# Kernel tuning notes

Measured on AMD Instinct MI355X. Metric: run time of the kernel, lower is better.

The kernel has to match this reference:

```python
import jax, jax.numpy as jnp
import numpy as np

N = 100000      # nodes
D = 128         # in_channels
P = 64          # num_prompts
E = 3_200_000   # graph edges
EPT = 5_000_000 # kNN prompt-graph edges (k=50)
EPS = 0.1       # ot_epsilon
ITERS = 20      # sinkhorn max_iters


def _l2norm(x):
    # F.normalize(p=2, dim=1) with eps=1e-12
    return x / jnp.maximum(jnp.linalg.norm(x, axis=1, keepdims=True), 1e-12)


def setup_inputs() -> dict:
    key = jax.random.key(0)
    k1, k2, k3, k4, k5 = jax.random.split(key, 5)
    x = jax.random.normal(k1, (N, D), dtype=jnp.float32)
    edge_index = jax.random.randint(k2, (2, E), 0, N, dtype=jnp.int32)
    edge_weight = jax.random.uniform(k3, (E,), dtype=jnp.float32)
    pt_edge_index = jax.random.randint(k4, (2, EPT), 0, N, dtype=jnp.int32)
    # xavier_uniform for prompt_tokens
    bound = float(np.sqrt(6.0 / (P + D)))
    prompt_tokens = jax.random.uniform(k5, (P, D), dtype=jnp.float32, minval=-bound, maxval=bound)
    alpha_feat = jnp.float32(0.01)
    gamma = jnp.float32(0.5)
    return {"x": x, "edge_index": edge_index, "edge_weight": edge_weight,
            "pt_edge_index": pt_edge_index, "prompt_tokens": prompt_tokens,
            "alpha_feat": alpha_feat, "gamma": gamma}


def reference(x, edge_index, edge_weight, pt_edge_index, prompt_tokens, alpha_feat, gamma):
    n = x.shape[0]
    row, col = edge_index[0], edge_index[1]
    # degree of col (unweighted count), GCN-style symmetric normalization
    deg = jax.ops.segment_sum(jnp.ones_like(edge_weight), col, num_segments=n)
    deg_inv_sqrt = jnp.where(deg > 0, deg ** -0.5, 0.0)
    norm_weight = deg_inv_sqrt[row] * edge_weight * deg_inv_sqrt[col]  # [E]
    # scatter-add aggregation: x_aggr[row] += x[col] * norm_weight
    x_aggr = jax.ops.segment_sum(x[col] * norm_weight[:, None], row, num_segments=n)
    x_struct = (1.0 - gamma) * x + gamma * x_aggr

    xs = _l2norm(x_struct)               # [N, D]
    pn = _l2norm(prompt_tokens)          # [P, D]

    # Sinkhorn OT: cost = 1 - cosine sim, uniform marginals
    C = 1.0 - xs @ pn.T                  # [N, P]
    K = jnp.exp(-C / EPS)
    p = prompt_tokens.shape[0]
    a = jnp.full((n,), 1.0 / n, dtype=x.dtype)
    b = jnp.full((p,), 1.0 / p, dtype=x.dtype)
    u = a
    for _ in range(ITERS):
        v = b / (K.T @ u + 1e-30)
        u = a / (K @ v + 1e-30)
    T_star = u[:, None] * K * v[None, :]  # [N, P]
    ot_loss = jnp.sum(T_star * C)

    prompt_message = n * (T_star @ prompt_tokens)  # [N, D]
    x_adapted = x + alpha_feat * prompt_message

    xf = _l2norm(x_adapted)
    pt_row, pt_col = pt_edge_index[0], pt_edge_index[1]
    w = jnp.sum(xf[pt_row] * xf[pt_col], axis=1)   # [EPT]
    w = jax.nn.relu(w)
    w = w / (jnp.max(w) + 1e-8)
    return (x_adapted, ot_loss, w)
```

## Files before the change

kernel.cpp:

```cpp
#include <hip/hip_runtime.h>
#include <stdint.h>

#define D_DIM 128
#define P_DIM 64

#define O_CNTR   0x000000ull
#define O_CNTC   0x080000ull
#define O_DIS    0x100000ull
#define O_ROWPTR 0x180000ull
#define O_CURSOR 0x200000ull
#define O_PART   0x280000ull
#define O_KT     0x290000ull
#define O_MAXW   0x2A0000ull
#define O_PNT    0x2B0000ull
#define O_U      0x300000ull
#define O_CSRC   0x400000ull
#define O_CSRW   0x1040000ull
#define O_XF     0x400000ull
#define O_K      0x1C80000ull

__device__ __forceinline__ float wsumf(float v){
  #pragma unroll
  for (int d=1; d<64; d<<=1) v += __shfl_xor(v, d);
  return v;
}

__device__ __forceinline__ unsigned f2bf(float f){
  unsigned u = __float_as_uint(f);
  return (u + 0x7fffu + ((u>>16)&1u)) >> 16;
}

__device__ __forceinline__ float dp2(unsigned a, unsigned b){
  float al = __uint_as_float(a<<16),  ah = __uint_as_float(a & 0xffff0000u);
  float bl = __uint_as_float(b<<16),  bh = __uint_as_float(b & 0xffff0000u);
  return al*bl + ah*bh;
}

__global__ void k_zero(int* cntr, int* cntc, float* kt, unsigned* maxw, float* loss_slot, int n){
  int i = blockIdx.x*blockDim.x + threadIdx.x;
  int st = gridDim.x*blockDim.x;
  for (int j=i; j<n; j+=st){ cntr[j]=0; cntc[j]=0; }
  for (int j=i; j<21*64; j+=st) kt[j]=0.f;
  if (i==0){ *maxw = 0u; *loss_slot = 0.f; }
}

__global__ void k_deg(const int* __restrict__ ei, int E, int* cntr, int* cntc){
  int i = blockIdx.x*blockDim.x + threadIdx.x;
  int st = gridDim.x*blockDim.x;
  for (int e=i; e<E; e+=st){
    atomicAdd(&cntr[ei[e]], 1);
    atomicAdd(&cntc[ei[E+e]], 1);
  }
}

__global__ void k_deginv(const int* __restrict__ cntc, float* __restrict__ dis, int n){
  int i = blockIdx.x*blockDim.x + threadIdx.x;
  if (i < n){
    int c = cntc[i];
    dis[i] = (c > 0) ? rsqrtf((float)c) : 0.f;
  }
}

__global__ void k_scan_a(const int* __restrict__ cnt, int* __restrict__ part, int n){
  __shared__ int sm[4];
  int base = blockIdx.x*1024;
  int t = threadIdx.x;
  int s = 0;
  #pragma unroll
  for (int k=0;k<4;k++){ int idx = base + t + 256*k; if (idx<n) s += cnt[idx]; }
  #pragma unroll
  for (int d=1; d<64; d<<=1) s += __shfl_xor(s, d);
  if ((t&63)==0) sm[t>>6] = s;
  __syncthreads();
  if (t==0) part[blockIdx.x] = sm[0]+sm[1]+sm[2]+sm[3];
}

__global__ void k_scan_b(int* part, int nb, int* row_ptr, int n, int E){
  if (threadIdx.x==0 && blockIdx.x==0){
    int run = 0;
    for (int i=0;i<nb;i++){ int v = part[i]; part[i] = run; run += v; }
    row_ptr[n] = E;
  }
}

__global__ void k_scan_c(const int* __restrict__ cnt, const int* __restrict__ part,
                         int* __restrict__ row_ptr, int* __restrict__ cursor, int n){
  __shared__ int warp_tot[4];
  int base = blockIdx.x*1024;
  int t = threadIdx.x;
  int lane = t&63, wv = t>>6;
  int v[4];
  #pragma unroll
  for (int k=0;k<4;k++){ int idx = base + t*4 + k; v[k] = (idx<n) ? cnt[idx] : 0; }
  int local = v[0]+v[1]+v[2]+v[3];
  int sc = local;
  #pragma unroll
  for (int d=1; d<64; d<<=1){ int y = __shfl_up(sc, d); if (lane>=d) sc += y; }
  if (lane==63) warp_tot[wv] = sc;
  __syncthreads();
  int woff = 0;
  for (int i=0;i<wv;i++) woff += warp_tot[i];
  int run = part[blockIdx.x] + woff + (sc - local);
  #pragma unroll
  for (int k=0;k<4;k++){
    int idx = base + t*4 + k;
    if (idx<n){ row_ptr[idx] = run; cursor[idx] = run; run += v[k]; }
  }
}

__global__ void k_prep_pn(const float* __restrict__ pt, float* __restrict__ pnT){
  int r = blockIdx.x;
  int l = threadIdx.x;
  float2 v = ((const float2*)pt)[r*64 + l];
  float ss = wsumf(v.x*v.x + v.y*v.y);
  float inv = 1.f / fmaxf(sqrtf(ss), 1e-12f);
  pnT[(2*l)*64   + r] = v.x*inv;
  pnT[(2*l+1)*64 + r] = v.y*inv;
}

__global__ void k_scatter(const int* __restrict__ ei, const float* __restrict__ ew,
                          const float* __restrict__ dis, int* cursor,
                          int* __restrict__ csr_col, float* __restrict__ csr_w, int E){
  int i = blockIdx.x*blockDim.x + threadIdx.x;
  int st = gridDim.x*blockDim.x;
  for (int e=i; e<E; e+=st){
    int r = ei[e], c = ei[E+e];
    float w = dis[r]*ew[e]*dis[c];
    int pos = atomicAdd(&cursor[r], 1);
    csr_col[pos] = c; csr_w[pos] = w;
  }
}

__global__ __launch_bounds__(256) void k_struct(const float* __restrict__ x,
    const int* __restrict__ row_ptr, const int* __restrict__ csr_col,
    const float* __restrict__ csr_w, const float* __restrict__ pnT_g,
    const float* __restrict__ gamma_p, float* __restrict__ Km, int n){
  __shared__ __align__(16) float pnT[128*64];
  __shared__ __align__(16) float xsrow[4][128];
  for (int i=threadIdx.x; i<128*64; i+=256) pnT[i] = pnT_g[i];
  __syncthreads();
  float g = *gamma_p, om = 1.f - g;
  int lane = threadIdx.x&63, wv = threadIdx.x>>6;
  int wid = blockIdx.x*4 + wv, nw = gridDim.x*4;
  for (int r=wid; r<n; r+=nw){
    int e0 = row_ptr[r], e1 = row_ptr[r+1];
    float ax=0.f, ay=0.f;
    for (int e=e0; e<e1; e++){
      int c = csr_col[e]; float w = csr_w[e];
      float2 xv = ((const float2*)x)[(size_t)c*64 + lane];
      ax = fmaf(w, xv.x, ax); ay = fmaf(w, xv.y, ay);
    }
    float2 xr = ((const float2*)x)[(size_t)r*64 + lane];
    float sx = om*xr.x + g*ax;
    float sy = om*xr.y + g*ay;
    float ss = wsumf(sx*sx + sy*sy);
    float inv = 1.f / fmaxf(sqrtf(ss), 1e-12f);
    xsrow[wv][2*lane]   = sx*inv;
    xsrow[wv][2*lane+1] = sy*inv;
    float acc = 0.f;
    #pragma unroll
    for (int d=0; d<128; d++) acc = fmaf(xsrow[wv][d], pnT[d*64+lane], acc);
    Km[(size_t)r*64 + lane] = exp2f((acc - 1.f) * 14.426950408889634f);
  }
}

__global__ __launch_bounds__(256) void k_colsum(const float* __restrict__ Km,
                                                float* __restrict__ kt_out, int n){
  __shared__ float ktsh[64];
  int tid = threadIdx.x;
  if (tid<64) ktsh[tid] = 0.f;
  __syncthreads();
  int lane = tid&63, wv = tid>>6, sub = lane>>4, li = lane&15;
  float4 acc = make_float4(0,0,0,0);
  int wid = blockIdx.x*4 + wv, nw = gridDim.x*4;
  for (int base=wid*4; base<n; base+=nw*4){
    int r = base + sub;
    if (r<n){
      float4 kv = ((const float4*)(Km + (size_t)r*64))[li];
      acc.x += kv.x; acc.y += kv.y; acc.z += kv.z; acc.w += kv.w;
    }
  }
  acc.x += __shfl_xor(acc.x,16); acc.x += __shfl_xor(acc.x,32);
  acc.y += __shfl_xor(acc.y,16); acc.y += __shfl_xor(acc.y,32);
  acc.z += __shfl_xor(acc.z,16); acc.z += __shfl_xor(acc.z,32);
  acc.w += __shfl_xor(acc.w,16); acc.w += __shfl_xor(acc.w,32);
  if (sub==0){
    atomicAdd(&ktsh[li*4+0], acc.x);
    atomicAdd(&ktsh[li*4+1], acc.y);
    atomicAdd(&ktsh[li*4+2], acc.z);
    atomicAdd(&ktsh[li*4+3], acc.w);
  }
  __syncthreads();
  float anorm = 1.0f/(float)n;
  if (tid<64) atomicAdd(&kt_out[tid], ktsh[tid]*anorm);
}

__global__ __launch_bounds__(256) void k_sink(const float* __restrict__ Km,
    const float* __restrict__ kt_in, float* __restrict__ kt_out,
    float* __restrict__ u, int n){
  __shared__ __align__(16) float vsh[64];
  __shared__ float ktsh[64];
  int tid = threadIdx.x;
  if (tid<64){ vsh[tid] = (1.0f/64.0f)/(kt_in[tid] + 1e-30f); ktsh[tid] = 0.f; }
  __syncthreads();
  int lane = tid&63, wv = tid>>6, sub = lane>>4, li = lane&15;
  float4 vv = ((const float4*)vsh)[li];
  float anorm = 1.0f/(float)n;
  float4 acc = make_float4(0,0,0,0);
  int wid = blockIdx.x*4 + wv, nw = gridDim.x*4;
  for (int base=wid*4; base<n; base+=nw*4){
    int r = base + sub;
    float4 kv = make_float4(0,0,0,0);
    if (r<n) kv = ((const float4*)(Km + (size_t)r*64))[li];
    float d = kv.x*vv.x + kv.y*vv.y + kv.z*vv.z + kv.w*vv.w;
    d += __shfl_xor(d,1); d += __shfl_xor(d,2); d += __shfl_xor(d,4); d += __shfl_xor(d,8);
    float un = anorm/(d + 1e-30f);
    if (li==0 && r<n) u[r] = un;
    acc.x = fmaf(kv.x, un, acc.x);
    acc.y = fmaf(kv.y, un, acc.y);
    acc.z = fmaf(kv.z, un, acc.z);
    acc.w = fmaf(kv.w, un, acc.w);
  }
  acc.x += __shfl_xor(acc.x,16); acc.x += __shfl_xor(acc.x,32);
  acc.y += __shfl_xor(acc.y,16); acc.y += __shfl_xor(acc.y,32);
  acc.z += __shfl_xor(acc.z,16); acc.z += __shfl_xor(acc.z,32);
  acc.w += __shfl_xor(acc.w,16); acc.w += __shfl_xor(acc.w,32);
  if (sub==0){
    atomicAdd(&ktsh[li*4+0], acc.x);
    atomicAdd(&ktsh[li*4+1], acc.y);
    atomicAdd(&ktsh[li*4+2], acc.z);
    atomicAdd(&ktsh[li*4+3], acc.w);
  }
  __syncthreads();
  if (tid<64) atomicAdd(&kt_out[tid], ktsh[tid]);
}

__global__ __launch_bounds__(256) void k_final(const float* __restrict__ x,
    const float* __restrict__ Km, const float* __restrict__ u,
    const float* __restrict__ kt19, const float* __restrict__ pt,
    const float* __restrict__ alpha_p, float* __restrict__ out_x,
    float* __restrict__ out_loss, unsigned* __restrict__ xf, int n){
  __shared__ __align__(16) float pts[64*128];
  __shared__ float trow[4][64];
  __shared__ float vsh[64];
  __shared__ float blockloss;
  int tid = threadIdx.x;
  for (int i=tid; i<8192; i+=256) pts[i] = pt[i];
  if (tid<64) vsh[tid] = (1.0f/64.0f)/(kt19[tid] + 1e-30f);
  if (tid==0) blockloss = 0.f;
  __syncthreads();
  float alpha = *alpha_p;
  float coeff = alpha*(float)n;
  int lane = tid&63, wv = tid>>6;
  int wid = blockIdx.x*4 + wv, nw = gridDim.x*4;
  float lossacc = 0.f;
  for (int r=wid; r<n; r+=nw){
    float kv = Km[(size_t)r*64 + lane];
    float T = u[r]*kv*vsh[lane];
    float C = log2f(kv) * (-0.069314718055994531f);
    lossacc = fmaf(T, C, lossacc);
    trow[wv][lane] = T;
    float m0=0.f, m1=0.f;
    #pragma unroll
    for (int p=0; p<64; p++){
      float t = trow[wv][p];
      float2 pv = ((const float2*)pts)[p*64 + lane];
      m0 = fmaf(t, pv.x, m0); m1 = fmaf(t, pv.y, m1);
    }
    float2 xr = ((const float2*)x)[(size_t)r*64 + lane];
    float ox = fmaf(coeff, m0, xr.x);
    float oy = fmaf(coeff, m1, xr.y);
    ((float2*)out_x)[(size_t)r*64 + lane] = make_float2(ox, oy);
    float ss = wsumf(ox*ox + oy*oy);
    float inv = 1.f / fmaxf(sqrtf(ss), 1e-12f);
    unsigned lo = f2bf(ox*inv), hi = f2bf(oy*inv);
    xf[(size_t)r*64 + lane] = lo | (hi<<16);
  }
  lossacc = wsumf(lossacc);
  if (lane==0) atomicAdd(&blockloss, lossacc);
  __syncthreads();
  if (tid==0) atomicAdd(out_loss, blockloss);
}

__global__ __launch_bounds__(256) void k_edge(const int* __restrict__ pte,
    const unsigned* __restrict__ xf, float* __restrict__ wout,
    unsigned* __restrict__ maxw, int ept){
  __shared__ unsigned blockmax;
  if (threadIdx.x==0) blockmax = 0u;
  __syncthreads();
  int lane = threadIdx.x&63, wv = threadIdx.x>>6, sub = lane>>4, li = lane&15;
  int wid = blockIdx.x*4 + wv, nw = gridDim.x*4;
  float lm = 0.f;
  for (int base=wid*4; base<ept; base+=nw*4){
    int e = base + sub;
    float dot = 0.f;
    if (e<ept){
      int r = pte[e], c = pte[ept+e];
      uint4 A = *(((const uint4*)(xf + (size_t)r*64)) + li);
      uint4 B = *(((const uint4*)(xf + (size_t)c*64)) + li);
      dot = dp2(A.x,B.x) + dp2(A.y,B.y) + dp2(A.z,B.z) + dp2(A.w,B.w);
    }
    dot += __shfl_xor(dot,1); dot += __shfl_xor(dot,2);
    dot += __shfl_xor(dot,4); dot += __shfl_xor(dot,8);
    if (li==0 && e<ept){
      float w = fmaxf(dot, 0.f);
      wout[e] = w;
      lm = fmaxf(lm, w);
    }
  }
  #pragma unroll
  for (int d=1; d<64; d<<=1) lm = fmaxf(lm, __shfl_xor(lm, d));
  if (lane==0) atomicMax(&blockmax, __float_as_uint(lm));
  __syncthreads();
  if (threadIdx.x==0) atomicMax(maxw, blockmax);
}

__global__ void k_normw(float* __restrict__ w, const unsigned* __restrict__ maxw, int ept){
  float inv = 1.f/(__uint_as_float(*maxw) + 1e-8f);
  int i = blockIdx.x*blockDim.x + threadIdx.x;
  int st = gridDim.x*blockDim.x;
  for (int e=i; e<ept; e+=st) w[e] *= inv;
}

extern "C" void kernel_launch(void* const* d_in, const int* in_sizes, int n_in,
                              void* d_out, int out_size, void* d_ws, size_t ws_size,
                              hipStream_t stream){
  const float* x       = (const float*)d_in[0];
  const int*   ei      = (const int*)  d_in[1];
  const float* ew      = (const float*)d_in[2];
  const int*   pte     = (const int*)  d_in[3];
  const float* pt      = (const float*)d_in[4];
  const float* alpha_p = (const float*)d_in[5];
  const float* gamma_p = (const float*)d_in[6];
  int n   = in_sizes[0] / D_DIM;
  int E   = in_sizes[1] / 2;
  int ept = in_sizes[3] / 2;

  char* ws = (char*)d_ws;
  int*      cntr    = (int*)     (ws + O_CNTR);
  int*      cntc    = (int*)     (ws + O_CNTC);
  float*    dis     = (float*)   (ws + O_DIS);
  int*      row_ptr = (int*)     (ws + O_ROWPTR);
  int*      cursor  = (int*)     (ws + O_CURSOR);
  int*      part    = (int*)     (ws + O_PART);
  float*    kt      = (float*)   (ws + O_KT);
  unsigned* maxw    = (unsigned*)(ws + O_MAXW);
  float*    pnT     = (float*)   (ws + O_PNT);
  float*    ubuf    = (float*)   (ws + O_U);
  int*      csrc    = (int*)     (ws + O_CSRC);
  float*    csrw    = (float*)   (ws + O_CSRW);
  unsigned* xf      = (unsigned*)(ws + O_XF);
  float*    Km      = (float*)   (ws + O_K);

  float* out_x    = (float*)d_out;
  float* out_loss = (float*)d_out + (size_t)n*D_DIM;
  float* out_w    = out_loss + 1;

  int nb = (n + 1023)/1024;

  k_zero   <<<512, 256, 0, stream>>>(cntr, cntc, kt, maxw, out_loss, n);
  k_deg    <<<2048, 256, 0, stream>>>(ei, E, cntr, cntc);
  k_deginv <<<(n+255)/256, 256, 0, stream>>>(cntc, dis, n);
  k_scan_a <<<nb, 256, 0, stream>>>(cntr, part, n);
  k_scan_b <<<1, 64, 0, stream>>>(part, nb, row_ptr, n, E);
  k_scan_c <<<nb, 256, 0, stream>>>(cntr, part, row_ptr, cursor, n);
  k_prep_pn<<<64, 64, 0, stream>>>(pt, pnT);
  k_scatter<<<2048, 256, 0, stream>>>(ei, ew, dis, cursor, csrc, csrw, E);
  k_struct <<<2048, 256, 0, stream>>>(x, row_ptr, csrc, csrw, pnT, gamma_p, Km, n);
  k_colsum <<<1024, 256, 0, stream>>>(Km, kt, n);
  for (int t=1; t<=20; t++)
    k_sink <<<1024, 256, 0, stream>>>(Km, kt + (t-1)*64, kt + t*64, ubuf, n);
  k_final  <<<2048, 256, 0, stream>>>(x, Km, ubuf, kt + 19*64, pt, alpha_p,
                                      out_x, out_loss, xf, n);
  k_edge   <<<4096, 256, 0, stream>>>(pte, xf, out_w, maxw, ept);
  k_normw  <<<2048, 256, 0, stream>>>(out_w, maxw, ept);
}
```

Before: 2.167 ms.

## Fuse column sum into struct kernel, interleave CSR, bf16 prompts, XCD-local row partitioning

```diff
diff --git a/kernel.cpp b/kernel.cpp
--- a/kernel.cpp
+++ b/kernel.cpp
@@ -12,10 +12,9 @@
 #define O_PART   0x280000ull
 #define O_KT     0x290000ull
 #define O_MAXW   0x2A0000ull
-#define O_PNT    0x2B0000ull
+#define O_PNB    0x2B0000ull
 #define O_U      0x300000ull
-#define O_CSRC   0x400000ull
-#define O_CSRW   0x1040000ull
+#define O_CSR    0x400000ull
 #define O_XF     0x400000ull
 #define O_K      0x1C80000ull
 
@@ -30,10 +29,11 @@
   return (u + 0x7fffu + ((u>>16)&1u)) >> 16;
 }
 
+__device__ __forceinline__ float bflo(unsigned u){ return __uint_as_float(u<<16); }
+__device__ __forceinline__ float bfhi(unsigned u){ return __uint_as_float(u & 0xffff0000u); }
+
 __device__ __forceinline__ float dp2(unsigned a, unsigned b){
-  float al = __uint_as_float(a<<16),  ah = __uint_as_float(a & 0xffff0000u);
-  float bl = __uint_as_float(b<<16),  bh = __uint_as_float(b & 0xffff0000u);
-  return al*bl + ah*bh;
+  return bflo(a)*bflo(b) + bfhi(a)*bfhi(b);
 }
 
 __global__ void k_zero(int* cntr, int* cntc, float* kt, unsigned* maxw, float* loss_slot, int n){
@@ -108,49 +108,68 @@
   }
 }
 
-__global__ void k_prep_pn(const float* __restrict__ pt, float* __restrict__ pnT){
+__global__ void k_prep_pn(const float* __restrict__ pt, unsigned* __restrict__ pnb){
   int r = blockIdx.x;
   int l = threadIdx.x;
   float2 v = ((const float2*)pt)[r*64 + l];
   float ss = wsumf(v.x*v.x + v.y*v.y);
   float inv = 1.f / fmaxf(sqrtf(ss), 1e-12f);
-  pnT[(2*l)*64   + r] = v.x*inv;
-  pnT[(2*l+1)*64 + r] = v.y*inv;
+  pnb[l*64 + r] = f2bf(v.x*inv) | (f2bf(v.y*inv) << 16);
 }
 
 __global__ void k_scatter(const int* __restrict__ ei, const float* __restrict__ ew,
                           const float* __restrict__ dis, int* cursor,
-                          int* __restrict__ csr_col, float* __restrict__ csr_w, int E){
+                          uint2* __restrict__ csr, int E){
   int i = blockIdx.x*blockDim.x + threadIdx.x;
   int st = gridDim.x*blockDim.x;
   for (int e=i; e<E; e+=st){
     int r = ei[e], c = ei[E+e];
     float w = dis[r]*ew[e]*dis[c];
     int pos = atomicAdd(&cursor[r], 1);
-    csr_col[pos] = c; csr_w[pos] = w;
+    csr[pos] = make_uint2((unsigned)c, __float_as_uint(w));
   }
 }
 
 __global__ __launch_bounds__(256) void k_struct(const float* __restrict__ x,
-    const int* __restrict__ row_ptr, const int* __restrict__ csr_col,
-    const float* __restrict__ csr_w, const float* __restrict__ pnT_g,
-    const float* __restrict__ gamma_p, float* __restrict__ Km, int n){
-  __shared__ __align__(16) float pnT[128*64];
+    const int* __restrict__ row_ptr, const uint2* __restrict__ csr,
+    const unsigned* __restrict__ pnb_g, const float* __restrict__ gamma_p,
+    float* __restrict__ Km, float* __restrict__ kt0, int n){
+  __shared__ unsigned pnbs[64*64];
   __shared__ __align__(16) float xsrow[4][128];
-  for (int i=threadIdx.x; i<128*64; i+=256) pnT[i] = pnT_g[i];
+  __shared__ float ktsh[64];
+  int tid = threadIdx.x;
+  for (int i=tid; i<4096; i+=256) pnbs[i] = pnb_g[i];
+  if (tid<64) ktsh[tid] = 0.f;
   __syncthreads();
   float g = *gamma_p, om = 1.f - g;
-  int lane = threadIdx.x&63, wv = threadIdx.x>>6;
+  int lane = tid&63, wv = tid>>6;
   int wid = blockIdx.x*4 + wv, nw = gridDim.x*4;
+  const float2* X2 = (const float2*)x;
+  float kacc = 0.f;
   for (int r=wid; r<n; r+=nw){
     int e0 = row_ptr[r], e1 = row_ptr[r+1];
     float ax=0.f, ay=0.f;
-    for (int e=e0; e<e1; e++){
-      int c = csr_col[e]; float w = csr_w[e];
-      float2 xv = ((const float2*)x)[(size_t)c*64 + lane];
+    int e = e0;
+    for (; e+3 < e1; e += 4){
+      uint2 q0 = csr[e], q1 = csr[e+1], q2 = csr[e+2], q3 = csr[e+3];
+      float2 v0 = X2[(size_t)q0.x*64 + lane];
+      float2 v1 = X2[(size_t)q1.x*64 + lane];
+      float2 v2 = X2[(size_t)q2.x*64 + lane];
+      float2 v3 = X2[(size_t)q3.x*64 + lane];
+      float w0 = __uint_as_float(q0.y), w1 = __uint_as_float(q1.y);
+      float w2 = __uint_as_float(q2.y), w3 = __uint_as_float(q3.y);
+      ax = fmaf(w0, v0.x, ax); ay = fmaf(w0, v0.y, ay);
+      ax = fmaf(w1, v1.x, ax); ay = fmaf(w1, v1.y, ay);
+      ax = fmaf(w2, v2.x, ax); ay = fmaf(w2, v2.y, ay);
+      ax = fmaf(w3, v3.x, ax); ay = fmaf(w3, v3.y, ay);
+    }
+    for (; e < e1; e++){
+      uint2 q = csr[e];
+      float2 xv = X2[(size_t)q.x*64 + lane];
+      float w = __uint_as_float(q.y);
       ax = fmaf(w, xv.x, ax); ay = fmaf(w, xv.y, ay);
     }
-    float2 xr = ((const float2*)x)[(size_t)r*64 + lane];
+    float2 xr = X2[(size_t)r*64 + lane];
     float sx = om*xr.x + g*ax;
     float sy = om*xr.y + g*ay;
     float ss = wsumf(sx*sx + sy*sy);
@@ -159,40 +178,19 @@
     xsrow[wv][2*lane+1] = sy*inv;
     float acc = 0.f;
     #pragma unroll
-    for (int d=0; d<128; d++) acc = fmaf(xsrow[wv][d], pnT[d*64+lane], acc);
-    Km[(size_t)r*64 + lane] = exp2f((acc - 1.f) * 14.426950408889634f);
-  }
-}
-
-__global__ __launch_bounds__(256) void k_colsum(const float* __restrict__ Km,
-                                                float* __restrict__ kt_out, int n){
-  __shared__ float ktsh[64];
-  int tid = threadIdx.x;
-  if (tid<64) ktsh[tid] = 0.f;
-  __syncthreads();
-  int lane = tid&63, wv = tid>>6, sub = lane>>4, li = lane&15;
-  float4 acc = make_float4(0,0,0,0);
-  int wid = blockIdx.x*4 + wv, nw = gridDim.x*4;
-  for (int base=wid*4; base<n; base+=nw*4){
-    int r = base + sub;
-    if (r<n){
-      float4 kv = ((const float4*)(Km + (size_t)r*64))[li];
-      acc.x += kv.x; acc.y += kv.y; acc.z += kv.z; acc.w += kv.w;
-    }
-  }
-  acc.x += __shfl_xor(acc.x,16); acc.x += __shfl_xor(acc.x,32);
-  acc.y += __shfl_xor(acc.y,16); acc.y += __shfl_xor(acc.y,32);
-  acc.z += __shfl_xor(acc.z,16); acc.z += __shfl_xor(acc.z,32);
-  acc.w += __shfl_xor(acc.w,16); acc.w += __shfl_xor(acc.w,32);
-  if (sub==0){
-    atomicAdd(&ktsh[li*4+0], acc.x);
-    atomicAdd(&ktsh[li*4+1], acc.y);
-    atomicAdd(&ktsh[li*4+2], acc.z);
-    atomicAdd(&ktsh[li*4+3], acc.w);
-  }
-  __syncthreads();
-  float anorm = 1.0f/(float)n;
-  if (tid<64) atomicAdd(&kt_out[tid], ktsh[tid]*anorm);
+    for (int k=0; k<64; k++){
+      unsigned pp = pnbs[k*64 + lane];
+      float2 xv = *(const float2*)&xsrow[wv][2*k];
+      acc = fmaf(bflo(pp), xv.x, acc);
+      acc = fmaf(bfhi(pp), xv.y, acc);
+    }
+    float kv = exp2f((acc - 1.f) * 14.426950408889634f);
+    Km[(size_t)r*64 + lane] = kv;
+    kacc += kv;
+  }
+  atomicAdd(&ktsh[lane], kacc);
+  __syncthreads();
+  if (tid<64) atomicAdd(&kt0[tid], ktsh[tid] * (1.0f/(float)n));
 }
 
 __global__ __launch_bounds__(256) void k_sink(const float* __restrict__ Km,
@@ -207,15 +205,17 @@
   float4 vv = ((const float4*)vsh)[li];
   float anorm = 1.0f/(float)n;
   float4 acc = make_float4(0,0,0,0);
-  int wid = blockIdx.x*4 + wv, nw = gridDim.x*4;
-  for (int base=wid*4; base<n; base+=nw*4){
+  int xcd = blockIdx.x & 7, lb = blockIdx.x >> 3, nlb = gridDim.x >> 3;
+  int r0 = (int)((long long)xcd*n/8), r1 = (int)((long long)(xcd+1)*n/8);
+  int wid = lb*4 + wv, nw = nlb*4;
+  for (int base=r0+wid*4; base<r1; base+=nw*4){
     int r = base + sub;
     float4 kv = make_float4(0,0,0,0);
-    if (r<n) kv = ((const float4*)(Km + (size_t)r*64))[li];
+    if (r<r1) kv = ((const float4*)(Km + (size_t)r*64))[li];
     float d = kv.x*vv.x + kv.y*vv.y + kv.z*vv.z + kv.w*vv.w;
     d += __shfl_xor(d,1); d += __shfl_xor(d,2); d += __shfl_xor(d,4); d += __shfl_xor(d,8);
     float un = anorm/(d + 1e-30f);
-    if (li==0 && r<n) u[r] = un;
+    if (li==0 && r<r1) u[r] = un;
     acc.x = fmaf(kv.x, un, acc.x);
     acc.y = fmaf(kv.y, un, acc.y);
     acc.z = fmaf(kv.z, un, acc.z);
@@ -252,9 +252,11 @@
   float alpha = *alpha_p;
   float coeff = alpha*(float)n;
   int lane = tid&63, wv = tid>>6;
-  int wid = blockIdx.x*4 + wv, nw = gridDim.x*4;
+  int xcd = blockIdx.x & 7, lb = blockIdx.x >> 3, nlb = gridDim.x >> 3;
+  int r0 = (int)((long long)xcd*n/8), r1 = (int)((long long)(xcd+1)*n/8);
+  int wid = lb*4 + wv, nw = nlb*4;
   float lossacc = 0.f;
-  for (int r=wid; r<n; r+=nw){
+  for (int r=r0+wid; r<r1; r+=nw){
     float kv = Km[(size_t)r*64 + lane];
     float T = u[r]*kv*vsh[lane];
     float C = log2f(kv) * (-0.069314718055994531f);
@@ -291,21 +293,31 @@
   int lane = threadIdx.x&63, wv = threadIdx.x>>6, sub = lane>>4, li = lane&15;
   int wid = blockIdx.x*4 + wv, nw = gridDim.x*4;
   float lm = 0.f;
-  for (int base=wid*4; base<ept; base+=nw*4){
-    int e = base + sub;
-    float dot = 0.f;
-    if (e<ept){
-      int r = pte[e], c = pte[ept+e];
-      uint4 A = *(((const uint4*)(xf + (size_t)r*64)) + li);
-      uint4 B = *(((const uint4*)(xf + (size_t)c*64)) + li);
-      dot = dp2(A.x,B.x) + dp2(A.y,B.y) + dp2(A.z,B.z) + dp2(A.w,B.w);
-    }
-    dot += __shfl_xor(dot,1); dot += __shfl_xor(dot,2);
-    dot += __shfl_xor(dot,4); dot += __shfl_xor(dot,8);
-    if (li==0 && e<ept){
-      float w = fmaxf(dot, 0.f);
-      wout[e] = w;
-      lm = fmaxf(lm, w);
+  for (int base=wid*8; base<ept; base+=nw*8){
+    int eA = base + sub, eB = base + 4 + sub;
+    bool vA = eA < ept, vB = eB < ept;
+    float dA = 0.f, dB = 0.f;
+    uint4 A0, A1, B0, B1;
+    int rA=0,cA=0,rB=0,cB=0;
+    if (vA){ rA = pte[eA]; cA = pte[ept+eA]; }
+    if (vB){ rB = pte[eB]; cB = pte[ept+eB]; }
+    if (vA){
+      A0 = *(((const uint4*)(xf + (size_t)rA*64)) + li);
+      A1 = *(((const uint4*)(xf + (size_t)cA*64)) + li);
+    }
+    if (vB){
+      B0 = *(((const uint4*)(xf + (size_t)rB*64)) + li);
+      B1 = *(((const uint4*)(xf + (size_t)cB*64)) + li);
+    }
+    if (vA) dA = dp2(A0.x,A1.x) + dp2(A0.y,A1.y) + dp2(A0.z,A1.z) + dp2(A0.w,A1.w);
+    if (vB) dB = dp2(B0.x,B1.x) + dp2(B0.y,B1.y) + dp2(B0.z,B1.z) + dp2(B0.w,B1.w);
+    dA += __shfl_xor(dA,1); dB += __shfl_xor(dB,1);
+    dA += __shfl_xor(dA,2); dB += __shfl_xor(dB,2);
+    dA += __shfl_xor(dA,4); dB += __shfl_xor(dB,4);
+    dA += __shfl_xor(dA,8); dB += __shfl_xor(dB,8);
+    if (li==0){
+      if (vA){ float w = fmaxf(dA, 0.f); wout[eA] = w; lm = fmaxf(lm, w); }
+      if (vB){ float w = fmaxf(dB, 0.f); wout[eB] = w; lm = fmaxf(lm, w); }
     }
   }
   #pragma unroll
@@ -345,10 +357,9 @@
   int*      part    = (int*)     (ws + O_PART);
   float*    kt      = (float*)   (ws + O_KT);
   unsigned* maxw    = (unsigned*)(ws + O_MAXW);
-  float*    pnT     = (float*)   (ws + O_PNT);
+  unsigned* pnb     = (unsigned*)(ws + O_PNB);
   float*    ubuf    = (float*)   (ws + O_U);
-  int*      csrc    = (int*)     (ws + O_CSRC);
-  float*    csrw    = (float*)   (ws + O_CSRW);
+  uint2*    csr     = (uint2*)   (ws + O_CSR);
   unsigned* xf      = (unsigned*)(ws + O_XF);
   float*    Km      = (float*)   (ws + O_K);
 
@@ -364,10 +375,9 @@
   k_scan_a <<<nb, 256, 0, stream>>>(cntr, part, n);
   k_scan_b <<<1, 64, 0, stream>>>(part, nb, row_ptr, n, E);
   k_scan_c <<<nb, 256, 0, stream>>>(cntr, part, row_ptr, cursor, n);
-  k_prep_pn<<<64, 64, 0, stream>>>(pt, pnT);
-  k_scatter<<<2048, 256, 0, stream>>>(ei, ew, dis, cursor, csrc, csrw, E);
-  k_struct <<<2048, 256, 0, stream>>>(x, row_ptr, csrc, csrw, pnT, gamma_p, Km, n);
-  k_colsum <<<1024, 256, 0, stream>>>(Km, kt, n);
+  k_prep_pn<<<64, 64, 0, stream>>>(pt, pnb);
+  k_scatter<<<2048, 256, 0, stream>>>(ei, ew, dis, cursor, csr, E);
+  k_struct <<<2048, 256, 0, stream>>>(x, row_ptr, csr, pnb, gamma_p, Km, kt, n);
   for (int t=1; t<=20; t++)
     k_sink <<<1024, 256, 0, stream>>>(Km, kt + (t-1)*64, kt + t*64, ubuf, n);
   k_final  <<<2048, 256, 0, stream>>>(x, Km, ubuf, kt + 19*64, pt, alpha_p,
```

New measurement: 1.942 ms. -10.4%, faster.
